# Performance work log

Measured on AMD Instinct MI355X. Metric: run time of the kernel, lower is better.

Reference implementation:

```python
import jax, jax.numpy as jnp
import numpy as np

B, N, C, H = 8, 1024, 768, 12
D = C // H  # 64
LAMBDA_INIT = 0.8 - 0.6 * np.exp(-0.3 * (1 - 1))  # layer_idx=1 -> 0.2
EPS = 1e-5


def setup_inputs() -> dict:
    key = jax.random.key(0)
    ks = jax.random.split(key, 8)
    s = 0.02
    return {
        "x": jax.random.normal(ks[0], (B, N, C), dtype=jnp.float32),
        "Wq": jax.random.normal(ks[1], (C, 2 * C), dtype=jnp.float32) * s,
        "Wk": jax.random.normal(ks[2], (C, 2 * C), dtype=jnp.float32) * s,
        "Wv": jax.random.normal(ks[3], (C, 2 * C), dtype=jnp.float32) * s,
        "lam": jnp.float32(1.0),
        "gamma": jnp.ones((2 * D,), dtype=jnp.float32),
        "beta": jnp.zeros((2 * D,), dtype=jnp.float32),
        "Wp": jax.random.normal(ks[4], (2 * C, C), dtype=jnp.float32) * s,
        "bp": jnp.zeros((C,), dtype=jnp.float32),
    }


def reference(x, Wq, Wk, Wv, lam, gamma, beta, Wp, bp):
    scale = D ** -0.5
    # project to double-width qkv, split heads: (B, H, N, 2D)
    q = (x @ Wq).reshape(B, N, H, 2 * D).transpose(0, 2, 1, 3)
    k = (x @ Wk).reshape(B, N, H, 2 * D).transpose(0, 2, 1, 3)
    v = (x @ Wv).reshape(B, N, H, 2 * D).transpose(0, 2, 1, 3)
    q1, q2 = jnp.split(q, 2, axis=-1)
    k1, k2 = jnp.split(k, 2, axis=-1)
    a1 = jax.nn.softmax(jnp.einsum("bhnd,bhmd->bhnm", q1, k1) * scale, axis=-1)
    a2 = jax.nn.softmax(jnp.einsum("bhnd,bhmd->bhnm", q2, k2) * scale, axis=-1)
    # lambda-weighted differential attention, then apply to double-width V
    out = jnp.einsum("bhnm,bhmd->bhnd", a1 - lam * a2, v)  # (B, H, N, 2D)
    # LayerNorm over the 2D channel dim
    mu = out.mean(axis=-1, keepdims=True)
    var = out.var(axis=-1, keepdims=True)
    out = (out - mu) * jax.lax.rsqrt(var + EPS) * gamma + beta
    out = out * (1.0 - LAMBDA_INIT)
    out = out.transpose(0, 2, 1, 3).reshape(B, N, 2 * C)
    return out @ Wp + bp
```

## Files before the change

kernel.cpp:

```cpp
#include <hip/hip_runtime.h>

#define B_ 8
#define N_ 1024
#define C_ 768
#define H_ 12
#define BH_ 96
#define D2_ 128
#define C2_ 1536

static constexpr float SCALE_LOG2 = 0.125f * 1.4426950408889634f;
static constexpr float OUT_SCALE  = 0.8f;
static constexpr float EPS_       = 1e-5f;

using bf16x8 = __attribute__((ext_vector_type(8))) short;
using f32x4  = __attribute__((ext_vector_type(4))) float;
typedef unsigned short ushort_t;
typedef unsigned int   uint_t;

#define GLOAD16(g, l) __builtin_amdgcn_global_load_lds( \
    (const __attribute__((address_space(1))) void*)(g), \
    (__attribute__((address_space(3))) void*)(l), 16, 0, 0)

__device__ __forceinline__ ushort_t f2bf(float f) {
    uint_t u = __float_as_uint(f);
    u = (u + 0x7FFFu + ((u >> 16) & 1u)) >> 16;
    return (ushort_t)u;
}
__device__ __forceinline__ uint_t packbf(float a, float b) {
    return (uint_t)f2bf(a) | ((uint_t)f2bf(b) << 16);
}

__global__ __launch_bounds__(256) void cvt_bf16_kernel(const float* __restrict__ in,
                                                       ushort_t* __restrict__ out, int n4) {
    for (int i = blockIdx.x * 256 + threadIdx.x; i < n4; i += gridDim.x * 256) {
        float4 v = reinterpret_cast<const float4*>(in)[i];
        ushort4 o;
        o.x = f2bf(v.x); o.y = f2bf(v.y); o.z = f2bf(v.z); o.w = f2bf(v.w);
        reinterpret_cast<ushort4*>(out)[i] = o;
    }
}

__global__ __launch_bounds__(256) void transpose_cvt_kernel(const float* __restrict__ W,
                                                            ushort_t* __restrict__ Wt,
                                                            int K, int Nn) {
    __shared__ float t[32][33];
    const int n0 = blockIdx.x * 32, k0 = blockIdx.y * 32;
    const int tx = threadIdx.x & 31, ty = threadIdx.x >> 5;
    #pragma unroll
    for (int r = ty; r < 32; r += 8)
        t[r][tx] = W[(size_t)(k0 + r) * Nn + n0 + tx];
    __syncthreads();
    #pragma unroll
    for (int r = ty; r < 32; r += 8)
        Wt[(size_t)(n0 + r) * K + k0 + tx] = f2bf(t[tx][r]);
}

__global__ __launch_bounds__(256) void transpose_v_kernel(const ushort_t* __restrict__ V,
                                                          ushort_t* __restrict__ Vt) {
    __shared__ ushort_t t[64][65];
    const int bh = blockIdx.z;
    const int d0 = blockIdx.x * 64, n0 = blockIdx.y * 64;
    const int tx = threadIdx.x & 63, ty = threadIdx.x >> 6;
    const ushort_t* src = V + (size_t)bh * N_ * D2_;
    ushort_t* dst = Vt + (size_t)bh * N_ * D2_;
    #pragma unroll
    for (int r = ty; r < 64; r += 4)
        t[r][tx] = src[(size_t)(n0 + r) * D2_ + d0 + tx];
    __syncthreads();
    #pragma unroll
    for (int r = ty; r < 64; r += 4)
        dst[(size_t)(d0 + r) * N_ + n0 + tx] = t[tx][r];
}

template <int REMAP>
__global__ __launch_bounds__(256)
void gemm_bf16_kernel(const ushort_t* __restrict__ A, const ushort_t* __restrict__ Bt,
                      const float* __restrict__ bias, void* __restrict__ dst,
                      int M, int Nn, int K)
{
    __shared__ __align__(16) char As[8192];
    __shared__ __align__(16) char Bs[8192];
    const int tid = threadIdx.x;
    const int wv = tid >> 6, lane = tid & 63;
    const int l15 = lane & 15, lg = lane >> 4;
    const int m0 = blockIdx.y * 128, n0 = blockIdx.x * 128;
    const int wm = (wv >> 1) * 64, wn = (wv & 1) * 64;

    f32x4 acc[4][4] = {};
    const size_t ldb = (size_t)K * 2;

    for (int k0 = 0; k0 < K; k0 += 32) {
        __syncthreads();
        #pragma unroll
        for (int q = 0; q < 2; ++q) {
            const int o = wv * 2048 + q * 1024 + lane * 16;
            const int sw = (o & 63) ^ ((((o >> 7) & 3)) << 4);
            const char* sa = (const char*)A + (size_t)(m0 + (o >> 6)) * ldb + k0 * 2 + sw;
            const char* sb = (const char*)Bt + (size_t)(n0 + (o >> 6)) * ldb + k0 * 2 + sw;
            GLOAD16(sa, As + wv * 2048 + q * 1024);
            GLOAD16(sb, Bs + wv * 2048 + q * 1024);
        }
        __syncthreads();
        bf16x8 af[4], bfr[4];
        #pragma unroll
        for (int i = 0; i < 4; ++i) {
            const int ra = wm + i * 16 + l15;
            af[i] = *(const bf16x8*)(As + ra * 64 + ((lg ^ ((ra >> 1) & 3)) << 4));
            const int rb = wn + i * 16 + l15;
            bfr[i] = *(const bf16x8*)(Bs + rb * 64 + ((lg ^ ((rb >> 1) & 3)) << 4));
        }
        #pragma unroll
        for (int i = 0; i < 4; ++i)
            #pragma unroll
            for (int j = 0; j < 4; ++j)
                acc[i][j] = __builtin_amdgcn_mfma_f32_16x16x32_bf16(af[i], bfr[j], acc[i][j], 0, 0, 0);
    }

    if (REMAP) {
        ushort_t* D = (ushort_t*)dst;
        #pragma unroll
        for (int i = 0; i < 4; ++i)
            #pragma unroll
            for (int r = 0; r < 4; ++r) {
                const int m = m0 + wm + i * 16 + lg * 4 + r;
                const int b = m >> 10, ns = m & 1023;
                #pragma unroll
                for (int j = 0; j < 4; ++j) {
                    const int n = n0 + wn + j * 16 + l15;
                    const int h = n >> 7, d = n & 127;
                    D[(((size_t)(b * H_ + h)) * N_ + ns) * D2_ + d] = f2bf(acc[i][j][r]);
                }
            }
    } else {
        float* D = (float*)dst;
        #pragma unroll
        for (int i = 0; i < 4; ++i)
            #pragma unroll
            for (int r = 0; r < 4; ++r) {
                const int m = m0 + wm + i * 16 + lg * 4 + r;
                #pragma unroll
                for (int j = 0; j < 4; ++j) {
                    const int n = n0 + wn + j * 16 + l15;
                    D[(size_t)m * Nn + n] = acc[i][j][r] + bias[n];
                }
            }
    }
}

__global__ __launch_bounds__(256)
void attn_kernel(const ushort_t* __restrict__ qb, const ushort_t* __restrict__ kb,
                 const ushort_t* __restrict__ vt, const float* __restrict__ lamp,
                 const float* __restrict__ gamma, const float* __restrict__ beta,
                 ushort_t* __restrict__ Y)
{
    __shared__ __align__(16) char Ks[8192];
    __shared__ __align__(16) char Vs[8192];
    __shared__ __align__(16) ushort_t Ps[4][2][16 * 40];

    const int tid = threadIdx.x;
    const int wv = tid >> 6, lane = tid & 63;
    const int l15 = lane & 15, lg = lane >> 4;
    const int bh = blockIdx.x >> 4;
    const int qt = blockIdx.x & 15;

    const char* kbase = (const char*)kb + (size_t)bh * (N_ * D2_ * 2);
    const char* vbase = (const char*)vt + (size_t)bh * (N_ * D2_ * 2);

    const int qrow = qt * 64 + wv * 16 + l15;
    const ushort_t* qptr = qb + (size_t)bh * N_ * D2_ + (size_t)qrow * D2_;
    bf16x8 Qf[4];
    #pragma unroll
    for (int c = 0; c < 4; ++c)
        Qf[c] = *(const bf16x8*)(qptr + c * 32 + lg * 8);

    f32x4 O1[8] = {}, O2[8] = {};
    float l1p = 0.f, l2p = 0.f;

    for (int t = 0; t < 32; ++t) {
        __syncthreads();
        #pragma unroll
        for (int q = 0; q < 2; ++q) {
            const int o = wv * 2048 + q * 1024 + lane * 16;
            const char* ks = kbase + t * 8192 + (o ^ ((((o >> 8) & 7)) << 4));
            GLOAD16(ks, Ks + wv * 2048 + q * 1024);
            const char* vs = vbase + (size_t)(o >> 6) * (N_ * 2) + t * 64
                           + ((o & 63) ^ ((((o >> 7) & 3)) << 4));
            GLOAD16(vs, Vs + wv * 2048 + q * 1024);
        }
        __syncthreads();

        f32x4 s1[2], s2[2];
        #pragma unroll
        for (int u = 0; u < 2; ++u) {
            const int row = u * 16 + l15;
            const char* kp = Ks + row * 256;
            bf16x8 k0 = *(const bf16x8*)(kp + (((0  + lg) ^ (row & 7)) << 4));
            bf16x8 k1 = *(const bf16x8*)(kp + (((4  + lg) ^ (row & 7)) << 4));
            bf16x8 k2 = *(const bf16x8*)(kp + (((8  + lg) ^ (row & 7)) << 4));
            bf16x8 k3 = *(const bf16x8*)(kp + (((12 + lg) ^ (row & 7)) << 4));
            f32x4 z = {0.f, 0.f, 0.f, 0.f};
            s1[u] = __builtin_amdgcn_mfma_f32_16x16x32_bf16(k0, Qf[0], z, 0, 0, 0);
            s1[u] = __builtin_amdgcn_mfma_f32_16x16x32_bf16(k1, Qf[1], s1[u], 0, 0, 0);
            s2[u] = __builtin_amdgcn_mfma_f32_16x16x32_bf16(k2, Qf[2], z, 0, 0, 0);
            s2[u] = __builtin_amdgcn_mfma_f32_16x16x32_bf16(k3, Qf[3], s2[u], 0, 0, 0);
        }

        float lp1 = 0.f, lp2 = 0.f;
        #pragma unroll
        for (int u = 0; u < 2; ++u) {
            const uint_t base = (uint_t)(l15 * 40 + u * 16 + lg * 4) >> 1;
            float a0 = exp2f(s1[u][0] * SCALE_LOG2), a1 = exp2f(s1[u][1] * SCALE_LOG2);
            float a2 = exp2f(s1[u][2] * SCALE_LOG2), a3 = exp2f(s1[u][3] * SCALE_LOG2);
            lp1 += (a0 + a1) + (a2 + a3);
            ((uint_t*)Ps[wv][0])[base]     = packbf(a0, a1);
            ((uint_t*)Ps[wv][0])[base + 1] = packbf(a2, a3);
            float b0 = exp2f(s2[u][0] * SCALE_LOG2), b1 = exp2f(s2[u][1] * SCALE_LOG2);
            float b2 = exp2f(s2[u][2] * SCALE_LOG2), b3 = exp2f(s2[u][3] * SCALE_LOG2);
            lp2 += (b0 + b1) + (b2 + b3);
            ((uint_t*)Ps[wv][1])[base]     = packbf(b0, b1);
            ((uint_t*)Ps[wv][1])[base + 1] = packbf(b2, b3);
        }
        l1p += lp1; l2p += lp2;

        bf16x8 pa1 = *(const bf16x8*)&Ps[wv][0][l15 * 40 + lg * 8];
        bf16x8 pa2 = *(const bf16x8*)&Ps[wv][1][l15 * 40 + lg * 8];

        #pragma unroll
        for (int c = 0; c < 8; ++c) {
            const int dr = c * 16 + l15;
            bf16x8 vf = *(const bf16x8*)(Vs + dr * 64 + ((lg ^ ((dr >> 1) & 3)) << 4));
            O1[c] = __builtin_amdgcn_mfma_f32_16x16x32_bf16(pa1, vf, O1[c], 0, 0, 0);
            O2[c] = __builtin_amdgcn_mfma_f32_16x16x32_bf16(pa2, vf, O2[c], 0, 0, 0);
        }
    }

    float l1 = l1p + __shfl_xor(l1p, 16); l1 += __shfl_xor(l1, 32);
    float l2 = l2p + __shfl_xor(l2p, 16); l2 += __shfl_xor(l2, 32);
    const float lam = lamp[0];
    float i1[4], i2[4];
    #pragma unroll
    for (int r = 0; r < 4; ++r) {
        i1[r] = 1.f / __shfl(l1, lg * 4 + r);
        i2[r] = lam / __shfl(l2, lg * 4 + r);
    }
    float su[4] = {0.f, 0.f, 0.f, 0.f}, sq[4] = {0.f, 0.f, 0.f, 0.f};
    float ov[8][4];
    #pragma unroll
    for (int c = 0; c < 8; ++c)
        #pragma unroll
        for (int r = 0; r < 4; ++r) {
            const float v = O1[c][r] * i1[r] - O2[c][r] * i2[r];
            ov[c][r] = v; su[r] += v; sq[r] += v * v;
        }
    #pragma unroll
    for (int r = 0; r < 4; ++r) {
        #pragma unroll
        for (int msk = 1; msk <= 8; msk <<= 1) {
            su[r] += __shfl_xor(su[r], msk);
            sq[r] += __shfl_xor(sq[r], msk);
        }
    }
    float gv[8], bv[8];
    #pragma unroll
    for (int c = 0; c < 8; ++c) { gv[c] = gamma[c * 16 + l15]; bv[c] = beta[c * 16 + l15]; }

    const int b = bh / H_, h = bh - (bh / H_) * H_;
    #pragma unroll
    for (int r = 0; r < 4; ++r) {
        const float mu = su[r] * (1.f / 128.f);
        const float var = sq[r] * (1.f / 128.f) - mu * mu;
        const float rstd = rsqrtf(var + EPS_);
        const int n = qt * 64 + wv * 16 + lg * 4 + r;
        ushort_t* yrow = Y + ((size_t)(b * N_ + n)) * C2_ + h * D2_;
        #pragma unroll
        for (int c = 0; c < 8; ++c) {
            const int d = c * 16 + l15;
            const float val = ((ov[c][r] - mu) * rstd * gv[c] + bv[c]) * OUT_SCALE;
            yrow[d] = f2bf(val);
        }
    }
}

extern "C" void kernel_launch(void* const* d_in, const int* in_sizes, int n_in,
                              void* d_out, int out_size, void* d_ws, size_t ws_size,
                              hipStream_t stream) {
    const float* x     = (const float*)d_in[0];
    const float* Wq    = (const float*)d_in[1];
    const float* Wk    = (const float*)d_in[2];
    const float* Wv    = (const float*)d_in[3];
    const float* lam   = (const float*)d_in[4];
    const float* gamma = (const float*)d_in[5];
    const float* beta  = (const float*)d_in[6];
    const float* Wp    = (const float*)d_in[7];
    const float* bp    = (const float*)d_in[8];
    float* out = (float*)d_out;

    char* w = (char*)d_ws;
    ushort_t* xb  = (ushort_t*)w;                 w += (size_t)B_ * N_ * C_ * 2;
    ushort_t* wqt = (ushort_t*)w;                 w += (size_t)C2_ * C_ * 2;
    ushort_t* wkt = (ushort_t*)w;                 w += (size_t)C2_ * C_ * 2;
    ushort_t* wvt = (ushort_t*)w;                 w += (size_t)C2_ * C_ * 2;
    ushort_t* wpt = (ushort_t*)w;                 w += (size_t)C_ * C2_ * 2;
    ushort_t* qbuf = (ushort_t*)w;                w += (size_t)BH_ * N_ * D2_ * 2;
    ushort_t* kbuf = (ushort_t*)w;                w += (size_t)BH_ * N_ * D2_ * 2;
    ushort_t* vbuf = (ushort_t*)w;                w += (size_t)BH_ * N_ * D2_ * 2;
    ushort_t* vtb  = (ushort_t*)w;                w += (size_t)BH_ * N_ * D2_ * 2;
    ushort_t* Yb   = (ushort_t*)w;                w += (size_t)B_ * N_ * C2_ * 2;

    const int M = B_ * N_;

    cvt_bf16_kernel<<<2048, 256, 0, stream>>>(x, xb, (B_ * N_ * C_) / 4);
    transpose_cvt_kernel<<<dim3(C2_ / 32, C_ / 32), 256, 0, stream>>>(Wq, wqt, C_, C2_);
    transpose_cvt_kernel<<<dim3(C2_ / 32, C_ / 32), 256, 0, stream>>>(Wk, wkt, C_, C2_);
    transpose_cvt_kernel<<<dim3(C2_ / 32, C_ / 32), 256, 0, stream>>>(Wv, wvt, C_, C2_);
    transpose_cvt_kernel<<<dim3(C_ / 32, C2_ / 32), 256, 0, stream>>>(Wp, wpt, C2_, C_);

    {
        dim3 grid(C2_ / 128, M / 128);
        gemm_bf16_kernel<1><<<grid, 256, 0, stream>>>(xb, wqt, nullptr, qbuf, M, C2_, C_);
        gemm_bf16_kernel<1><<<grid, 256, 0, stream>>>(xb, wkt, nullptr, kbuf, M, C2_, C_);
        gemm_bf16_kernel<1><<<grid, 256, 0, stream>>>(xb, wvt, nullptr, vbuf, M, C2_, C_);
    }
    transpose_v_kernel<<<dim3(D2_ / 64, N_ / 64, BH_), 256, 0, stream>>>(vbuf, vtb);

    attn_kernel<<<dim3(BH_ * (N_ / 64)), 256, 0, stream>>>(qbuf, kbuf, vtb, lam, gamma, beta, Yb);

    {
        dim3 grid(C_ / 128, M / 128);
        gemm_bf16_kernel<0><<<grid, 256, 0, stream>>>(Yb, wpt, bp, out, M, C_, C2_);
    }
}
```

Before: 338.8 us.

## Double-buffer K/V tiles with register prefetch and padded LDS in attention

Replaces the direct global-to-LDS loads, which needed two barriers per iteration, with register prefetch of the next K/V tile into a second LDS buffer. Global latency can then overlap with the MFMA work on the current tile, leaving one barrier per iteration. The XOR swizzle is replaced by row padding (272 and 80 bytes), and block indices are remapped so neighbouring blocks touch different heads. The cost is more LDS (double buffers plus padding), extra VGPRs for the prefetched data, and stores that now go through registers.

```diff
diff --git a/kernel.cpp b/kernel.cpp
--- a/kernel.cpp
+++ b/kernel.cpp
@@ -153,18 +153,29 @@
                  const float* __restrict__ gamma, const float* __restrict__ beta,
                  ushort_t* __restrict__ Y)
 {
-    __shared__ __align__(16) char Ks[8192];
-    __shared__ __align__(16) char Vs[8192];
+    __shared__ __align__(16) char Ks[2][32 * 272];
+    __shared__ __align__(16) char Vs[2][128 * 80];
     __shared__ __align__(16) ushort_t Ps[4][2][16 * 40];
 
     const int tid = threadIdx.x;
     const int wv = tid >> 6, lane = tid & 63;
     const int l15 = lane & 15, lg = lane >> 4;
-    const int bh = blockIdx.x >> 4;
-    const int qt = blockIdx.x & 15;
+    const int swz = (blockIdx.x & 7) * 192 + (blockIdx.x >> 3);
+    const int bh = swz >> 4;
+    const int qt = swz & 15;
 
     const char* kbase = (const char*)kb + (size_t)bh * (N_ * D2_ * 2);
     const char* vbase = (const char*)vt + (size_t)bh * (N_ * D2_ * 2);
+
+    const int krow = tid >> 4, kcol = tid & 15;
+    const int kg0 = tid * 16, kg1 = kg0 + 4096;
+    const int kw0 = krow * 272 + kcol * 16;
+    const int kw1 = (krow + 16) * 272 + kcol * 16;
+    const int vdr = tid >> 2, vpart = tid & 3;
+    const size_t vg0 = (size_t)vdr * (N_ * 2) + vpart * 16;
+    const size_t vg1 = (size_t)(vdr + 64) * (N_ * 2) + vpart * 16;
+    const int vw0 = vdr * 80 + vpart * 16;
+    const int vw1 = (vdr + 64) * 80 + vpart * 16;
 
     const int qrow = qt * 64 + wv * 16 + l15;
     const ushort_t* qptr = qb + (size_t)bh * N_ * D2_ + (size_t)qrow * D2_;
@@ -176,28 +187,38 @@
     f32x4 O1[8] = {}, O2[8] = {};
     float l1p = 0.f, l2p = 0.f;
 
+    {
+        uint4 a = *(const uint4*)(kbase + kg0);
+        uint4 b = *(const uint4*)(kbase + kg1);
+        uint4 c = *(const uint4*)(vbase + vg0);
+        uint4 d = *(const uint4*)(vbase + vg1);
+        *(uint4*)(Ks[0] + kw0) = a; *(uint4*)(Ks[0] + kw1) = b;
+        *(uint4*)(Vs[0] + vw0) = c; *(uint4*)(Vs[0] + vw1) = d;
+    }
+    __syncthreads();
+    int cur = 0;
+
     for (int t = 0; t < 32; ++t) {
-        __syncthreads();
-        #pragma unroll
-        for (int q = 0; q < 2; ++q) {
-            const int o = wv * 2048 + q * 1024 + lane * 16;
-            const char* ks = kbase + t * 8192 + (o ^ ((((o >> 8) & 7)) << 4));
-            GLOAD16(ks, Ks + wv * 2048 + q * 1024);
-            const char* vs = vbase + (size_t)(o >> 6) * (N_ * 2) + t * 64
-                           + ((o & 63) ^ ((((o >> 7) & 3)) << 4));
-            GLOAD16(vs, Vs + wv * 2048 + q * 1024);
-        }
-        __syncthreads();
+        uint4 nk0, nk1, nv0, nv1;
+        if (t < 31) {
+            nk0 = *(const uint4*)(kbase + (t + 1) * 8192 + kg0);
+            nk1 = *(const uint4*)(kbase + (t + 1) * 8192 + kg1);
+            nv0 = *(const uint4*)(vbase + vg0 + (t + 1) * 64);
+            nv1 = *(const uint4*)(vbase + vg1 + (t + 1) * 64);
+        }
+
+        const char* Kc = Ks[cur];
+        const char* Vc = Vs[cur];
 
         f32x4 s1[2], s2[2];
         #pragma unroll
         for (int u = 0; u < 2; ++u) {
             const int row = u * 16 + l15;
-            const char* kp = Ks + row * 256;
-            bf16x8 k0 = *(const bf16x8*)(kp + (((0  + lg) ^ (row & 7)) << 4));
-            bf16x8 k1 = *(const bf16x8*)(kp + (((4  + lg) ^ (row & 7)) << 4));
-            bf16x8 k2 = *(const bf16x8*)(kp + (((8  + lg) ^ (row & 7)) << 4));
-            bf16x8 k3 = *(const bf16x8*)(kp + (((12 + lg) ^ (row & 7)) << 4));
+            const char* kp = Kc + row * 272;
+            bf16x8 k0 = *(const bf16x8*)(kp + (0  + lg) * 16);
+            bf16x8 k1 = *(const bf16x8*)(kp + (4  + lg) * 16);
+            bf16x8 k2 = *(const bf16x8*)(kp + (8  + lg) * 16);
+            bf16x8 k3 = *(const bf16x8*)(kp + (12 + lg) * 16);
             f32x4 z = {0.f, 0.f, 0.f, 0.f};
             s1[u] = __builtin_amdgcn_mfma_f32_16x16x32_bf16(k0, Qf[0], z, 0, 0, 0);
             s1[u] = __builtin_amdgcn_mfma_f32_16x16x32_bf16(k1, Qf[1], s1[u], 0, 0, 0);
@@ -228,10 +249,19 @@
         #pragma unroll
         for (int c = 0; c < 8; ++c) {
             const int dr = c * 16 + l15;
-            bf16x8 vf = *(const bf16x8*)(Vs + dr * 64 + ((lg ^ ((dr >> 1) & 3)) << 4));
+            bf16x8 vf = *(const bf16x8*)(Vc + dr * 80 + lg * 16);
             O1[c] = __builtin_amdgcn_mfma_f32_16x16x32_bf16(pa1, vf, O1[c], 0, 0, 0);
             O2[c] = __builtin_amdgcn_mfma_f32_16x16x32_bf16(pa2, vf, O2[c], 0, 0, 0);
         }
+
+        if (t < 31) {
+            char* Kn = Ks[cur ^ 1];
+            char* Vn = Vs[cur ^ 1];
+            *(uint4*)(Kn + kw0) = nk0; *(uint4*)(Kn + kw1) = nk1;
+            *(uint4*)(Vn + vw0) = nv0; *(uint4*)(Vn + vw1) = nv1;
+        }
+        __syncthreads();
+        cur ^= 1;
     }
 
     float l1 = l1p + __shfl_xor(l1p, 16); l1 += __shfl_xor(l1, 32);
```

After: 314.7 us. 1.08x faster.
